# Performance work log

Measured on AMD Instinct MI355X. Metric: run time of the kernel, lower is better.

Reference implementation:

```python
import jax, jax.numpy as jnp
import numpy as np

# PointPillars KITTI config (matches init_kwargs)
VX, VY = 0.16, 0.16
PC_RANGE = (0.0, -39.68, -3.0, 69.12, 39.68, 1.0)
X_OFFSET = VX / 2 + PC_RANGE[0]          # 0.08
Y_OFFSET = VY / 2 + PC_RANGE[1]          # -39.60
Z_CONST = (PC_RANGE[5] + PC_RANGE[2]) / 2  # -1.0
GRID_X = int((PC_RANGE[3] - PC_RANGE[0]) / VX)  # 432
GRID_Y = int((PC_RANGE[4] - PC_RANGE[1]) / VY)  # 496
BN_EPS = 1e-3


def setup_inputs() -> dict:
    key = jax.random.key(0)
    ks = jax.random.split(key, 6)
    B, PPB, N, C = 4, 12000, 32, 64
    P = B * PPB
    # raw pillar point features (x,y,z,intensity)
    pillars = jax.random.normal(ks[0], (P, N, 4), dtype=jnp.float32)
    # unique pillar cells per batch element (real voxelization never duplicates cells)
    cells = jax.vmap(lambda k: jax.random.permutation(k, GRID_X * GRID_Y)[:PPB])(
        jax.random.split(ks[1], B))  # [B, PPB]
    coors_x = (cells // GRID_Y).reshape(-1).astype(jnp.int64)
    coors_y = (cells % GRID_Y).reshape(-1).astype(jnp.int64)
    coors_b = jnp.repeat(jnp.arange(B, dtype=jnp.int64), PPB)
    npoints = jax.random.randint(ks[2], (P,), 1, N + 1, dtype=jnp.int32)
    W = jax.random.normal(ks[3], (C, 10), dtype=jnp.float32) * 0.1
    gamma = jnp.ones((C,), dtype=jnp.float32)
    beta = jnp.zeros((C,), dtype=jnp.float32)
    return {"pillars": pillars, "W": W, "gamma": gamma, "beta": beta,
            "coors_x": coors_x, "coors_y": coors_y, "coors_b": coors_b,
            "npoints": npoints, "batch_size": B}


def reference(pillars, W, gamma, beta, coors_x, coors_y, coors_b, npoints, batch_size):
    dt = pillars.dtype
    P, N, _ = pillars.shape
    npf = npoints.astype(dt)
    # offset from pillar point-centroid (sum includes zero padding, as in torch)
    mean_xyz = jnp.sum(pillars[:, :, :3], axis=1, keepdims=True) / npf[:, None, None]
    off_center = pillars[:, :, :3] - mean_xyz  # [P,N,3]
    # offset from pillar cell center
    xo = pillars[:, :, 0:1] - (coors_x.astype(dt)[:, None, None] * VX + X_OFFSET)
    yo = pillars[:, :, 1:2] - (coors_y.astype(dt)[:, None, None] * VY + Y_OFFSET)
    zo = jnp.full_like(xo, Z_CONST)
    # features after the in-place overwrite of channels 0,1:
    # [x_off, y_off, z, intensity, dx, dy, dz, x_off, y_off, z_const]
    feats = jnp.concatenate(
        [xo, yo, pillars[:, :, 2:4], off_center, xo, yo, zo], axis=-1)  # [P,N,10]
    mask = (jnp.arange(N)[None, :] < npoints[:, None]).astype(dt)  # [P,N]
    feats = feats * mask[:, :, None]
    # per-point linear (no bias) -> BN (training-mode batch stats over P,N) -> ReLU
    x = jnp.einsum('pnf,cf->pnc', feats, W)  # [P,N,C]
    mu = jnp.mean(x, axis=(0, 1))
    var = jnp.var(x, axis=(0, 1))
    x = (x - mu) * jax.lax.rsqrt(var + BN_EPS) * gamma + beta
    x = jax.nn.relu(x)
    x_max = jnp.max(x, axis=1)  # [P,C] segment-max over points per pillar
    # scatter into dense BEV grid, then [B, C, Y, X]
    C = x_max.shape[-1]
    grid = jnp.zeros((batch_size, GRID_X, GRID_Y, C), dtype=dt)
    grid = grid.at[coors_b, coors_x, coors_y].set(x_max)
    return jnp.transpose(grid, (0, 3, 2, 1))
```

## Files before the change

kernel.cpp:

```cpp
#include <hip/hip_runtime.h>
#include <stdint.h>

#define GRID_X 432
#define GRID_Y 496
#define NB 4
#define NPTS 32
#define NC 64
#define NSLOTS 64
#define CELLS (GRID_Y * GRID_X)

constexpr float VXc = 0.16f, VYc = 0.16f;
constexpr float X_OFFSET = 0.08f, Y_OFFSET = -39.60f, Z_CONST = -1.0f;
constexpr float BN_EPS = 1e-3f;

__global__ __launch_bounds__(256) void pillar_stats_kernel(
    const float* __restrict__ pillars, const float* __restrict__ W,
    const int* __restrict__ cx, const int* __restrict__ cy,
    const int* __restrict__ cb, const int* __restrict__ npoints,
    float* __restrict__ vmax, float* __restrict__ vmin, int* __restrict__ map,
    double* __restrict__ dsum, double* __restrict__ dsq, int P)
{
    __shared__ float4 pts[4][NPTS];
    __shared__ float pinfo[4][4];
    __shared__ float ssum[4][NC], ssq[4][NC];

    const int tid = threadIdx.x;
    const int p0 = blockIdx.x * 4;

    if (tid < 128) {
        int pl = tid >> 5, n = tid & 31;
        int p = p0 + pl;
        float4 v = make_float4(0.f, 0.f, 0.f, 0.f);
        if (p < P) v = ((const float4*)pillars)[(size_t)p * NPTS + n];
        pts[pl][n] = v;
        float sx = v.x, sy = v.y, sz = v.z;
        #pragma unroll
        for (int m = 16; m >= 1; m >>= 1) {
            sx += __shfl_xor(sx, m, 32);
            sy += __shfl_xor(sy, m, 32);
            sz += __shfl_xor(sz, m, 32);
        }
        if (n == 0 && p < P) {
            float npf = (float)npoints[p];
            pinfo[pl][0] = sx / npf;
            pinfo[pl][1] = sy / npf;
            pinfo[pl][2] = sz / npf;
            pinfo[pl][3] = npf;
        }
    }
    if (tid >= 128 && tid < 132) {
        int p = p0 + (tid - 128);
        if (p < P) {
            int b = cb[p];
            map[(size_t)b * CELLS + (size_t)cy[p] * GRID_X + cx[p]] = p;
        }
    }
    __syncthreads();

    const int pl = tid >> 6, c = tid & 63;
    const int p = p0 + pl;
    float ssu = 0.f, sq2 = 0.f;
    if (p < P) {
        const float* w = W + c * 10;
        float w0 = w[0], w1 = w[1], w2 = w[2], w3 = w[3], w4 = w[4];
        float w5 = w[5], w6 = w[6], w7 = w[7], w8 = w[8], w9 = w[9];
        float Aw = w0 + w4 + w7;
        float Bw = w1 + w5 + w8;
        float Cw = w2 + w6;
        float Dw = w3;
        float cxo = cx[p] * VXc + X_OFFSET;
        float cyo = cy[p] * VYc + Y_OFFSET;
        float mx = pinfo[pl][0], my = pinfo[pl][1], mz = pinfo[pl][2];
        int np = (int)pinfo[pl][3];
        float E = -cxo * (w0 + w7) - cyo * (w1 + w8)
                  - mx * w4 - my * w5 - mz * w6 + Z_CONST * w9;
        float smax = -1e30f, smin = 1e30f;
        #pragma unroll
        for (int n = 0; n < NPTS; ++n) {
            float4 pt = pts[pl][n];
            float v = E;
            v = fmaf(pt.x, Aw, v);
            v = fmaf(pt.y, Bw, v);
            v = fmaf(pt.z, Cw, v);
            v = fmaf(pt.w, Dw, v);
            v = (n < np) ? v : 0.0f;
            smax = fmaxf(smax, v);
            smin = fminf(smin, v);
            ssu += v;
            sq2 = fmaf(v, v, sq2);
        }
        vmax[(size_t)p * NC + c] = smax;
        vmin[(size_t)p * NC + c] = smin;
    }
    ssum[pl][c] = ssu;
    ssq[pl][c]  = sq2;
    __syncthreads();
    if (tid < NC) {
        float s = ssum[0][tid] + ssum[1][tid] + ssum[2][tid] + ssum[3][tid];
        float q = ssq[0][tid]  + ssq[1][tid]  + ssq[2][tid]  + ssq[3][tid];
        int slot = blockIdx.x & (NSLOTS - 1);
        atomicAdd(&dsum[slot * NC + tid], (double)s);
        atomicAdd(&dsq[slot * NC + tid],  (double)q);
    }
}

__global__ void bn_params_kernel(const double* __restrict__ dsum,
                                 const double* __restrict__ dsq,
                                 const float* __restrict__ gamma,
                                 const float* __restrict__ beta,
                                 float* __restrict__ st, int P)
{
    int c = threadIdx.x;
    if (c < NC) {
        double s = 0.0, q = 0.0;
        for (int i = 0; i < NSLOTS; ++i) { s += dsum[i * NC + c]; q += dsq[i * NC + c]; }
        double cnt = (double)P * NPTS;
        double mu = s / cnt;
        double var = q / cnt - mu * mu;
        float scale = gamma[c] * (float)(1.0 / sqrt(var + (double)BN_EPS));
        float shift = beta[c] - (float)mu * scale;
        st[c] = scale;
        st[NC + c] = shift;
    }
}

__global__ __launch_bounds__(256) void scatter_out_kernel(
    const int* __restrict__ map, const float* __restrict__ vmax,
    const float* __restrict__ vmin, const float* __restrict__ st,
    float* __restrict__ out)
{
    const int q = blockIdx.x * 256 + threadIdx.x;
    const int b = blockIdx.y;
    const int m = map[(size_t)b * CELLS + q];
    float* ob = out + (size_t)b * NC * CELLS + q;
    #pragma unroll 8
    for (int c = 0; c < NC; ++c) {
        float r = 0.0f;
        if (m >= 0) {
            float s = st[c], t = st[NC + c];
            float v = (s >= 0.0f) ? vmax[(size_t)m * NC + c] : vmin[(size_t)m * NC + c];
            r = fmaxf(fmaf(s, v, t), 0.0f);
        }
        ob[(size_t)c * CELLS] = r;
    }
}

extern "C" void kernel_launch(void* const* d_in, const int* in_sizes, int n_in,
                              void* d_out, int out_size, void* d_ws, size_t ws_size,
                              hipStream_t stream) {
    const float* pillars = (const float*)d_in[0];
    const float* W       = (const float*)d_in[1];
    const float* gamma   = (const float*)d_in[2];
    const float* beta    = (const float*)d_in[3];
    const int*   cx      = (const int*)d_in[4];
    const int*   cy      = (const int*)d_in[5];
    const int*   cb      = (const int*)d_in[6];
    const int*   np      = (const int*)d_in[7];
    const int P = in_sizes[4];

    char* ws = (char*)d_ws;
    float* vmax = (float*)ws;
    float* vmin = vmax + (size_t)P * NC;
    int*   map  = (int*)(vmin + (size_t)P * NC);
    size_t mapN = (size_t)NB * CELLS;
    double* dsum = (double*)(((uintptr_t)(map + mapN) + 255) & ~(uintptr_t)255);
    double* dsq  = dsum + NSLOTS * NC;
    float*  st   = (float*)(dsq + NSLOTS * NC);

    hipMemsetAsync(map, 0xFF, mapN * sizeof(int), stream);
    hipMemsetAsync(dsum, 0, (size_t)NSLOTS * NC * 2 * sizeof(double), stream);

    pillar_stats_kernel<<<(P + 3) / 4, 256, 0, stream>>>(
        pillars, W, cx, cy, cb, np, vmax, vmin, map, dsum, dsq, P);
    bn_params_kernel<<<1, 64, 0, stream>>>(dsum, dsq, gamma, beta, st, P);
    scatter_out_kernel<<<dim3(CELLS / 256, NB), 256, 0, stream>>>(
        map, vmax, vmin, st, (float*)d_out);
}
```

Baseline: 287.0 us.

## Vectorize scatter output by four cells and process more pillars per stats block

The scatter kernel now handles four consecutive cells per thread. It reads the map as int4, writes float4 with nontemporal stores, and caches the BN scale/shift pairs in shared memory as float2. The stats kernel processes 16 pillars per block instead of 4, with each wave looping over four pillars. This reduces the number of blocks and the atomic traffic, and it hoists the weight loads. The gathers from vmax/vmin stay scattered, and per-thread work grows.

```diff
diff --git a/kernel.cpp b/kernel.cpp
--- a/kernel.cpp
+++ b/kernel.cpp
@@ -8,10 +8,15 @@
 #define NC 64
 #define NSLOTS 64
 #define CELLS (GRID_Y * GRID_X)
+#define QCELLS (CELLS / 4)
 
 constexpr float VXc = 0.16f, VYc = 0.16f;
 constexpr float X_OFFSET = 0.08f, Y_OFFSET = -39.60f, Z_CONST = -1.0f;
 constexpr float BN_EPS = 1e-3f;
+
+typedef float floatx4 __attribute__((ext_vector_type(4)));
+
+#define PPB 16
 
 __global__ __launch_bounds__(256) void pillar_stats_kernel(
     const float* __restrict__ pillars, const float* __restrict__ W,
@@ -20,16 +25,18 @@
     float* __restrict__ vmax, float* __restrict__ vmin, int* __restrict__ map,
     double* __restrict__ dsum, double* __restrict__ dsq, int P)
 {
-    __shared__ float4 pts[4][NPTS];
-    __shared__ float pinfo[4][4];
+    __shared__ float4 pts[PPB][NPTS];
+    __shared__ float pinfo[PPB][4];
     __shared__ float ssum[4][NC], ssq[4][NC];
 
     const int tid = threadIdx.x;
-    const int p0 = blockIdx.x * 4;
+    const int p0 = blockIdx.x * PPB;
 
-    if (tid < 128) {
-        int pl = tid >> 5, n = tid & 31;
-        int p = p0 + pl;
+    #pragma unroll
+    for (int pass = 0; pass < 2; ++pass) {
+        int pl = (tid >> 5) + pass * 8;
+        int n  = tid & 31;
+        int p  = p0 + pl;
         float4 v = make_float4(0.f, 0.f, 0.f, 0.f);
         if (p < P) v = ((const float4*)pillars)[(size_t)p * NPTS + n];
         pts[pl][n] = v;
@@ -48,8 +55,8 @@
             pinfo[pl][3] = npf;
         }
     }
-    if (tid >= 128 && tid < 132) {
-        int p = p0 + (tid - 128);
+    if (tid < PPB) {
+        int p = p0 + tid;
         if (p < P) {
             int b = cb[p];
             map[(size_t)b * CELLS + (size_t)cy[p] * GRID_X + cx[p]] = p;
@@ -57,43 +64,46 @@
     }
     __syncthreads();
 
-    const int pl = tid >> 6, c = tid & 63;
-    const int p = p0 + pl;
+    const int wv = tid >> 6, c = tid & 63;
+    const float* w = W + c * 10;
+    const float w0 = w[0], w1 = w[1], w2 = w[2], w3 = w[3], w4 = w[4];
+    const float w5 = w[5], w6 = w[6], w7 = w[7], w8 = w[8], w9 = w[9];
+    const float Aw = w0 + w4 + w7;
+    const float Bw = w1 + w5 + w8;
+    const float Cw = w2 + w6;
+    const float w07 = w0 + w7, w18 = w1 + w8;
     float ssu = 0.f, sq2 = 0.f;
-    if (p < P) {
-        const float* w = W + c * 10;
-        float w0 = w[0], w1 = w[1], w2 = w[2], w3 = w[3], w4 = w[4];
-        float w5 = w[5], w6 = w[6], w7 = w[7], w8 = w[8], w9 = w[9];
-        float Aw = w0 + w4 + w7;
-        float Bw = w1 + w5 + w8;
-        float Cw = w2 + w6;
-        float Dw = w3;
-        float cxo = cx[p] * VXc + X_OFFSET;
-        float cyo = cy[p] * VYc + Y_OFFSET;
-        float mx = pinfo[pl][0], my = pinfo[pl][1], mz = pinfo[pl][2];
-        int np = (int)pinfo[pl][3];
-        float E = -cxo * (w0 + w7) - cyo * (w1 + w8)
-                  - mx * w4 - my * w5 - mz * w6 + Z_CONST * w9;
-        float smax = -1e30f, smin = 1e30f;
-        #pragma unroll
-        for (int n = 0; n < NPTS; ++n) {
-            float4 pt = pts[pl][n];
-            float v = E;
-            v = fmaf(pt.x, Aw, v);
-            v = fmaf(pt.y, Bw, v);
-            v = fmaf(pt.z, Cw, v);
-            v = fmaf(pt.w, Dw, v);
-            v = (n < np) ? v : 0.0f;
-            smax = fmaxf(smax, v);
-            smin = fminf(smin, v);
-            ssu += v;
-            sq2 = fmaf(v, v, sq2);
+    #pragma unroll
+    for (int j = 0; j < 4; ++j) {
+        const int pl = wv * 4 + j;
+        const int p = p0 + pl;
+        if (p < P) {
+            float cxo = cx[p] * VXc + X_OFFSET;
+            float cyo = cy[p] * VYc + Y_OFFSET;
+            float mx = pinfo[pl][0], my = pinfo[pl][1], mz = pinfo[pl][2];
+            int npv = (int)pinfo[pl][3];
+            float E = -cxo * w07 - cyo * w18 - mx * w4 - my * w5 - mz * w6 + Z_CONST * w9;
+            float smax = -1e30f, smin = 1e30f;
+            #pragma unroll
+            for (int n = 0; n < NPTS; ++n) {
+                float4 pt = pts[pl][n];
+                float v = E;
+                v = fmaf(pt.x, Aw, v);
+                v = fmaf(pt.y, Bw, v);
+                v = fmaf(pt.z, Cw, v);
+                v = fmaf(pt.w, w3, v);
+                v = (n < npv) ? v : 0.0f;
+                smax = fmaxf(smax, v);
+                smin = fminf(smin, v);
+                ssu += v;
+                sq2 = fmaf(v, v, sq2);
+            }
+            vmax[(size_t)p * NC + c] = smax;
+            vmin[(size_t)p * NC + c] = smin;
         }
-        vmax[(size_t)p * NC + c] = smax;
-        vmin[(size_t)p * NC + c] = smin;
     }
-    ssum[pl][c] = ssu;
-    ssq[pl][c]  = sq2;
+    ssum[wv][c] = ssu;
+    ssq[wv][c]  = sq2;
     __syncthreads();
     if (tid < NC) {
         float s = ssum[0][tid] + ssum[1][tid] + ssum[2][tid] + ssum[3][tid];
@@ -108,7 +118,7 @@
                                  const double* __restrict__ dsq,
                                  const float* __restrict__ gamma,
                                  const float* __restrict__ beta,
-                                 float* __restrict__ st, int P)
+                                 float2* __restrict__ st, int P)
 {
     int c = threadIdx.x;
     if (c < NC) {
@@ -119,29 +129,34 @@
         double var = q / cnt - mu * mu;
         float scale = gamma[c] * (float)(1.0 / sqrt(var + (double)BN_EPS));
         float shift = beta[c] - (float)mu * scale;
-        st[c] = scale;
-        st[NC + c] = shift;
+        st[c] = make_float2(scale, shift);
     }
 }
 
 __global__ __launch_bounds__(256) void scatter_out_kernel(
     const int* __restrict__ map, const float* __restrict__ vmax,
-    const float* __restrict__ vmin, const float* __restrict__ st,
+    const float* __restrict__ vmin, const float2* __restrict__ st,
     float* __restrict__ out)
 {
-    const int q = blockIdx.x * 256 + threadIdx.x;
+    __shared__ float2 sst[NC];
+    if (threadIdx.x < NC) sst[threadIdx.x] = st[threadIdx.x];
+    __syncthreads();
+
+    const int q4 = blockIdx.x * 256 + threadIdx.x;
+    if (q4 >= QCELLS) return;
     const int b = blockIdx.y;
-    const int m = map[(size_t)b * CELLS + q];
-    float* ob = out + (size_t)b * NC * CELLS + q;
-    #pragma unroll 8
+    const int4 m = ((const int4*)(map + (size_t)b * CELLS))[q4];
+    floatx4* ob = (floatx4*)(out + (size_t)b * NC * CELLS) + q4;
+    #pragma unroll 4
     for (int c = 0; c < NC; ++c) {
-        float r = 0.0f;
-        if (m >= 0) {
-            float s = st[c], t = st[NC + c];
-            float v = (s >= 0.0f) ? vmax[(size_t)m * NC + c] : vmin[(size_t)m * NC + c];
-            r = fmaxf(fmaf(s, v, t), 0.0f);
-        }
-        ob[(size_t)c * CELLS] = r;
+        float2 s = sst[c];
+        const float* vs = (s.x >= 0.0f) ? vmax : vmin;
+        floatx4 r = (floatx4)(0.f);
+        if (m.x >= 0) r.x = fmaxf(fmaf(s.x, vs[(size_t)m.x * NC + c], s.y), 0.f);
+        if (m.y >= 0) r.y = fmaxf(fmaf(s.x, vs[(size_t)m.y * NC + c], s.y), 0.f);
+        if (m.z >= 0) r.z = fmaxf(fmaf(s.x, vs[(size_t)m.z * NC + c], s.y), 0.f);
+        if (m.w >= 0) r.w = fmaxf(fmaf(s.x, vs[(size_t)m.w * NC + c], s.y), 0.f);
+        __builtin_nontemporal_store(r, &ob[(size_t)c * QCELLS]);
     }
 }
 
@@ -165,14 +180,14 @@
     size_t mapN = (size_t)NB * CELLS;
     double* dsum = (double*)(((uintptr_t)(map + mapN) + 255) & ~(uintptr_t)255);
     double* dsq  = dsum + NSLOTS * NC;
-    float*  st   = (float*)(dsq + NSLOTS * NC);
+    float2* st   = (float2*)(dsq + NSLOTS * NC);
 
-    hipMemsetAsync(map, 0xFF, mapN * sizeof(int), stream);
-    hipMemsetAsync(dsum, 0, (size_t)NSLOTS * NC * 2 * sizeof(double), stream);
+    (void)hipMemsetAsync(map, 0xFF, mapN * sizeof(int), stream);
+    (void)hipMemsetAsync(dsum, 0, (size_t)NSLOTS * NC * 2 * sizeof(double), stream);
 
-    pillar_stats_kernel<<<(P + 3) / 4, 256, 0, stream>>>(
+    pillar_stats_kernel<<<(P + PPB - 1) / PPB, 256, 0, stream>>>(
         pillars, W, cx, cy, cb, np, vmax, vmin, map, dsum, dsq, P);
     bn_params_kernel<<<1, 64, 0, stream>>>(dsum, dsq, gamma, beta, st, P);
-    scatter_out_kernel<<<dim3(CELLS / 256, NB), 256, 0, stream>>>(
+    scatter_out_kernel<<<dim3((QCELLS + 255) / 256, NB), 256, 0, stream>>>(
         map, vmax, vmin, st, (float*)d_out);
 }
```

Result: no change. 288.5 us (+0.5%).
